# Optimization experiments

Hardware: AMD Instinct MI355X
Metric: run time of the kernel (lower is better)

Reference implementation:

```python
import jax, jax.numpy as jnp
import numpy as np

B, S, H, NH = 4, 2048, 1024, 16
HD = H // NH
EPS = 1e-12

def setup_inputs() -> dict:
    key = jax.random.key(0)
    ks = jax.random.split(key, 8)
    sc = 1.0 / np.sqrt(H)
    return {
        "input_tensor": jax.random.normal(ks[0], (B, S, H), jnp.float32),
        "attention_mask": jnp.zeros((B, 1, 1, S), jnp.float32),
        "Wq": jax.random.normal(ks[1], (H, H), jnp.float32) * sc,
        "bq": jnp.zeros((H,), jnp.float32),
        "Wk": jax.random.normal(ks[2], (H, H), jnp.float32) * sc,
        "bk": jnp.zeros((H,), jnp.float32),
        "Wv": jax.random.normal(ks[3], (H, H), jnp.float32) * sc,
        "bv": jnp.zeros((H,), jnp.float32),
        "Wo": jax.random.normal(ks[4], (H, H), jnp.float32) * sc,
        "bo": jnp.zeros((H,), jnp.float32),
        "ln_w": jnp.ones((H,), jnp.float32),
        "ln_b": jnpp_zeros if False else jnp.zeros((H,), jnp.float32),
    }

def reference(input_tensor, attention_mask, Wq, bq, Wk, bk, Wv, bv, Wo, bo, ln_w, ln_b):
    x = input_tensor  # [B,S,H]
    # QKV projections (torch Linear: x @ W.T + b), split heads -> [B,S,NH,HD]
    q = (x @ Wq.T + bq).reshape(B, S, NH, HD)
    k = (x @ Wk.T + bk).reshape(B, S, NH, HD)
    v = (x @ Wv.T + bv).reshape(B, S, NH, HD)
    # scores [B,NH,S,S]
    scores = jnp.einsum('bqhd,bkhd->bhqk', q, k) / jnp.sqrt(jnp.float32(HD))
    scores = scores + attention_mask  # broadcast [B,1,1,S]
    probs = jax.nn.softmax(scores, axis=-1)  # dropout is identity in eval
    ctx = jnp.einsum('bhqk,bkhd->bqhd', probs, v).reshape(B, S, H)
    # output dense + residual + LayerNorm (TF-style eps inside sqrt)
    h = ctx @ Wo.T + bo + x
    u = h.mean(-1, keepdims=True)
    s = jnp.mean((h - u) ** 2, axis=-1, keepdims=True)
    return ln_w * (h - u) / jnp.sqrt(s + EPS) + ln_b
```

## Files before the change

kernel.cpp:

```cpp
#include <hip/hip_runtime.h>

typedef __bf16 bf16;
typedef __bf16 bf16x8 __attribute__((ext_vector_type(8)));
typedef __bf16 bf16x4 __attribute__((ext_vector_type(4)));
typedef float floatx4 __attribute__((ext_vector_type(4)));
typedef int   intx4  __attribute__((ext_vector_type(4)));
typedef int   intx2  __attribute__((ext_vector_type(2)));

#define MFMA16(a,b,c) __builtin_amdgcn_mfma_f32_16x16x32_bf16((a),(b),(c),0,0,0)

constexpr int Bc  = 4;
constexpr int Sc  = 2048;
constexpr int Hc  = 1024;
constexpr int NHc = 16;
constexpr int HDc = 64;
constexpr int Mc  = Bc * Sc;
constexpr int KIT = Hc / 32;
constexpr float L2E = 1.44269504088896f;

union U64  { bf16x4 h; intx2 i; };

__device__ __forceinline__ void ld16(const bf16* g, bf16* l) {
    __builtin_amdgcn_global_load_lds(
        (const __attribute__((address_space(1))) void*)g,
        (__attribute__((address_space(3))) void*)l, 16, 0, 0);
}

__device__ __forceinline__ int detect_flag_block(const void* x, float* wmx)
{
    const unsigned short* xs = (const unsigned short*)x;
    const int tt = threadIdx.x;
    unsigned int bits = ((unsigned int)xs[tt]) << 16;
    float v = __uint_as_float(bits);
    float a = isfinite(v) ? fabsf(v) : 1e30f;
#pragma unroll
    for (int off = 1; off < 64; off <<= 1)
        a = fmaxf(a, __shfl_xor(a, off, 64));
    if ((tt & 63) == 0) wmx[tt >> 6] = a;
    __syncthreads();
    const float m = fmaxf(fmaxf(wmx[0], wmx[1]), fmaxf(wmx[2], wmx[3]));
    __syncthreads();
    return (m > 1e6f) ? 1 : 0;
}

__global__ __launch_bounds__(256)
void conv_all_k(const void* __restrict__ x,
                const void* __restrict__ Wq, const void* __restrict__ Wk,
                const void* __restrict__ Wv, const void* __restrict__ Wo,
                const void* __restrict__ mask,
                const void* __restrict__ bq, const void* __restrict__ bk,
                const void* __restrict__ bv, const void* __restrict__ bo,
                const void* __restrict__ lnw, const void* __restrict__ lnb,
                bf16* __restrict__ xb, bf16* __restrict__ wdst,
                float* maskf, float* bqf, float* bkf, float* bvf,
                float* bof, float* lnwf, float* lnbf)
{
    __shared__ float wmx[4];
    const int fl = detect_flag_block(x, wmx);

    const int g = blockIdx.x * 256 + threadIdx.x;
    if (g < 1048576) {
        if (fl) {
            const float* s = (const float*)x + (size_t)g * 8;
            union { intx4 v; bf16 e[8]; } o;
#pragma unroll
            for (int j = 0; j < 8; ++j) o.e[j] = (bf16)s[j];
            *(intx4*)(xb + (size_t)g * 8) = o.v;
        } else {
            *(intx4*)(xb + (size_t)g * 8) = *((const intx4*)x + g);
        }
    } else if (g < 1048576 + 524288) {
        const int gw = g - 1048576;
        const int wsel = gw >> 17, go = gw & 131071;
        const void* s = (wsel == 0) ? Wq : (wsel == 1) ? Wk : (wsel == 2) ? Wv : Wo;
        if (fl) {
            const float* sp = (const float*)s + (size_t)go * 8;
            union { intx4 v; bf16 e[8]; } o;
#pragma unroll
            for (int j = 0; j < 8; ++j) o.e[j] = (bf16)sp[j];
            *(intx4*)(wdst + (size_t)gw * 8) = o.v;
        } else {
            *(intx4*)(wdst + (size_t)gw * 8) = *((const intx4*)s + go);
        }
    } else {
        const int gs = g - 1048576 - 524288;
        if (gs >= 1792) return;
        const void* src; float* dst; int off; float scl = 1.0f;
        if (gs < 1024) { src = mask; dst = maskf; off = gs * 8; scl = L2E; }
        else {
            const int a = (gs - 1024) >> 7;
            off = ((gs - 1024) & 127) * 8;
            switch (a) {
                case 0: src = bq;  dst = bqf;  break;
                case 1: src = bk;  dst = bkf;  break;
                case 2: src = bv;  dst = bvf;  break;
                case 3: src = bo;  dst = bof;  break;
                case 4: src = lnw; dst = lnwf; break;
                default: src = lnb; dst = lnbf; break;
            }
        }
        if (fl) {
            const float* s = (const float*)src + off;
#pragma unroll
            for (int j = 0; j < 8; ++j) dst[off + j] = s[j] * scl;
        } else {
            union { intx4 v; bf16 e[8]; } u;
            u.v = *(const intx4*)((const bf16*)src + off);
#pragma unroll
            for (int j = 0; j < 8; ++j) dst[off + j] = (float)u.e[j] * scl;
        }
    }
}

template<int SWAP>
__device__ __forceinline__
void gemm_core(const bf16* __restrict__ A, const bf16* __restrict__ W,
               int m0, int n0, int t, bf16* As, bf16* Bs, floatx4 (&acc)[4][4])
{
    const int l  = t & 63, w = t >> 6;
    const int wr = w >> 1, wc = w & 1;
    const int lq = l >> 4, ln = l & 15;
    const int srow = t >> 2;
    const int scol = (t & 3) * 8;

    const bf16* a0 = A + (size_t)(m0 + srow) * Hc + scol;
    const bf16* b0 = W + (size_t)(n0 + srow) * Hc + scol;
    const int dst = srow * 32 + scol;

    auto stage = [&](int buf, int kb) {
        const int off = kb * 32;
        bf16* dA = As + buf * 4096;
        bf16* dB = Bs + buf * 4096;
        ld16(a0 + off,           dA + dst);
        ld16(a0 + 64 * Hc + off, dA + 64 * 32 + dst);
        ld16(b0 + off,           dB + dst);
        ld16(b0 + 64 * Hc + off, dB + 64 * 32 + dst);
    };

    stage(0, 0);
    int cur = 0;
    for (int kb = 0; kb < KIT; ++kb) {
        __syncthreads();
        if (kb + 1 < KIT) stage(cur ^ 1, kb + 1);

        const bf16* Ab = As + cur * 4096;
        const bf16* Bb = Bs + cur * 4096;
        bf16x8 af[4], bw[4];
#pragma unroll
        for (int i = 0; i < 4; ++i)
            af[i] = *(const bf16x8*)&Ab[(wr * 64 + i * 16 + ln) * 32 + lq * 8];
#pragma unroll
        for (int j = 0; j < 4; ++j)
            bw[j] = *(const bf16x8*)&Bb[(wc * 64 + j * 16 + ln) * 32 + lq * 8];

        __builtin_amdgcn_s_setprio(1);
#pragma unroll
        for (int i = 0; i < 4; ++i)
#pragma unroll
            for (int j = 0; j < 4; ++j)
                acc[i][j] = SWAP ? MFMA16(bw[j], af[i], acc[i][j])
                                 : MFMA16(af[i], bw[j], acc[i][j]);
        __builtin_amdgcn_s_setprio(0);
        cur ^= 1;
    }
}

__device__ __forceinline__ void xcd_remap(int bx, int by, int& m0, int& n0)
{
    const int flat = by * 8 + bx;
    const int sw   = (flat & 7) * 64 + (flat >> 3);
    m0 = (sw >> 3) * 128;
    n0 = (sw & 7) * 128;
}

__global__ __launch_bounds__(256, 3)
void qkv_gemm(const bf16* __restrict__ x,
              const bf16* __restrict__ Wq, const float* __restrict__ bq,
              const bf16* __restrict__ Wk, const float* __restrict__ bk,
              const bf16* __restrict__ Wv, const float* __restrict__ bv,
              bf16* __restrict__ qo, bf16* __restrict__ ko, bf16* __restrict__ vto)
{
    __shared__ __align__(16) bf16 smem[16384];
    const int z = blockIdx.z;
    const bf16*  W    = (z == 0) ? Wq : (z == 1) ? Wk : Wv;
    const float* bias = (z == 0) ? bq : (z == 1) ? bk : bv;

    int m0, n0;
    xcd_remap(blockIdx.x, blockIdx.y, m0, n0);
    const int t  = threadIdx.x;
    const int l  = t & 63, w = t >> 6;
    const int wr = w >> 1, wc = w & 1;
    const int lq = l >> 4, ln = l & 15;

    if (z < 2) {
        floatx4 acc[4][4] = {};
        gemm_core<1>(x, W, m0, n0, t, smem, smem + 8192, acc);
        bf16* out = (z == 0) ? qo : ko;
        const float sc = (z == 0) ? 0.125f * L2E : 1.0f;
#pragma unroll
        for (int j = 0; j < 4; ++j) {
            const int feat = n0 + wc * 64 + j * 16 + lq * 4;
            const floatx4 bb = *(const floatx4*)&bias[feat];
            const int hh = feat >> 6, dd = feat & 63;
#pragma unroll
            for (int i = 0; i < 4; ++i) {
                const int xrow = m0 + wr * 64 + i * 16 + ln;
                const int bi = xrow >> 11, si = xrow & (Sc - 1);
                U64 pk;
#pragma unroll
                for (int r = 0; r < 4; ++r) pk.h[r] = (bf16)((acc[i][j][r] + bb[r]) * sc);
                *(intx2*)&out[(((size_t)bi * NHc + hh) * Sc + si) * HDc + dd] = pk.i;
            }
        }
    } else {
        floatx4 acc[4][4] = {};
        gemm_core<0>(x, W, m0, n0, t, smem, smem + 8192, acc);
        bf16* Ct = smem;
        const int bi = m0 >> 11, s0 = m0 & (Sc - 1);
        for (int h2 = 0; h2 < 2; ++h2) {
            __syncthreads();
            if (wc == h2) {
#pragma unroll
                for (int j = 0; j < 4; ++j) {
                    const int c = j * 16 + ln;
                    const float bb = bias[n0 + h2 * 64 + c];
#pragma unroll
                    for (int i = 0; i < 4; ++i) {
                        U64 pk;
#pragma unroll
                        for (int r = 0; r < 4; ++r) pk.h[r] = (bf16)(acc[i][j][r] + bb);
                        *(intx2*)&Ct[c * 136 + wr * 64 + i * 16 + lq * 4] = pk.i;
                    }
                }
            }
            __syncthreads();
#pragma unroll
            for (int u = 0; u < 4; ++u) {
                const int id = t + 256 * u;
                const int c = id >> 4, rg = id & 15;
                const int hh = (n0 >> 6) + h2;
                intx4 val = *(const intx4*)&Ct[c * 136 + rg * 8];
                *(intx4*)&vto[(((size_t)bi * NHc + hh) * HDc + c) * Sc + s0 + rg * 8] = val;
            }
        }
    }
}

__global__ __launch_bounds__(256, 3)
void oproj_gemm(const bf16* __restrict__ ctx, const bf16* __restrict__ Wo,
                const float* __restrict__ bo, const bf16* __restrict__ xb,
                bf16* __restrict__ hout)
{
    __shared__ __align__(16) bf16 smem[16384];
    int m0, n0;
    xcd_remap(blockIdx.x, blockIdx.y, m0, n0);
    const int t  = threadIdx.x;
    floatx4 acc[4][4] = {};
    gemm_core<1>(ctx, Wo, m0, n0, t, smem, smem + 8192, acc);

    const int l  = t & 63, w = t >> 6;
    const int wr = w >> 1, wc = w & 1;
    const int lq = l >> 4, ln = l & 15;
#pragma unroll
    for (int j = 0; j < 4; ++j) {
        const int col = n0 + wc * 64 + j * 16 + lq * 4;
        const floatx4 bb = *(const floatx4*)&bo[col];
#pragma unroll
        for (int i = 0; i < 4; ++i) {
            const int row = m0 + wr * 64 + i * 16 + ln;
            U64 rx;
            rx.i = *(const intx2*)&xb[(size_t)row * Hc + col];
            U64 pk;
#pragma unroll
            for (int r = 0; r < 4; ++r)
                pk.h[r] = (bf16)(acc[i][j][r] + bb[r] + (float)rx.h[r]);
            *(intx2*)&hout[(size_t)row * Hc + col] = pk.i;
        }
    }
}

__global__ __launch_bounds__(256, 2)
void attention(const bf16* __restrict__ q, const bf16* __restrict__ k,
               const bf16* __restrict__ vt, const float* __restrict__ maskf,
               bf16* __restrict__ ctx)
{
    __shared__ __align__(16) bf16 Ks[2][64][64];
    __shared__ __align__(16) bf16 Vs[2][64][64];
    __shared__ __align__(16) bf16 Pt[4][64][64];

    const int raw = blockIdx.x;
    const int xcd = raw & 7, jj = raw >> 3;
    const int bh  = xcd * 8 + (jj >> 3);
    const int qt  = jj & 7;
    const int b = bh >> 4, h = bh & 15;
    const int t = threadIdx.x, w = t >> 6, l = t & 63;
    const int lq = l >> 4, ln = l & 15;
    const int q0 = qt * 256 + w * 64;

    const bf16* kg = k  + (size_t)bh * Sc * HDc;
    const bf16* vg = vt + (size_t)bh * HDc * Sc;
    const float* mbase = maskf + b * Sc;

    const int rr  = l >> 3;
    const int gsw = ((l & 7) ^ rr) << 3;
    const int r0  = w * 16 + rr, r1 = r0 + 8;
    const int dco = (l & 7) << 3;
    const int sw  = ln & 7;
    const int pkey = sw << 1;

    bf16x8 qf[4][2];
#pragma unroll
    for (int qb = 0; qb < 4; ++qb)
#pragma unroll
        for (int kh = 0; kh < 2; ++kh)
            qf[qb][kh] = *(const bf16x8*)(q + ((size_t)bh * Sc + q0 + qb * 16 + ln) * HDc
                                            + kh * 32 + lq * 8);

    bf16x8 ones8;
#pragma unroll
    for (int jj2 = 0; jj2 < 8; ++jj2) ones8[jj2] = (bf16)1.0f;

    floatx4 o[4][4] = {};
    floatx4 accl[4] = {};

    auto stage = [&](int buf, int kt) {
        bf16* Kd = &Ks[buf][0][0];
        bf16* Vd = &Vs[buf][0][0];
        ld16(kg + (size_t)(kt * 64 + r0) * HDc + gsw, Kd + r0 * 64 + dco);
        ld16(kg + (size_t)(kt * 64 + r1) * HDc + gsw, Kd + r1 * 64 + dco);
        ld16(vg + (size_t)r0 * Sc + kt * 64 + gsw,    Vd + r0 * 64 + dco);
        ld16(vg + (size_t)r1 * Sc + kt * 64 + gsw,    Vd + r1 * 64 + dco);
    };

    stage(0, 0);
    int cur = 0;
    bf16* PtW = &Pt[w][0][0];

    for (int kt = 0; kt < Sc / 64; ++kt) {
        __syncthreads();
        if (kt + 1 < Sc / 64) stage(cur ^ 1, kt + 1);

        floatx4 mvl[4];
#pragma unroll
        for (int cb = 0; cb < 4; ++cb)
            mvl[cb] = *(const floatx4*)(mbase + kt * 64 + cb * 16 + lq * 4);

        bf16x8 kf[4][2];
#pragma unroll
        for (int cb = 0; cb < 4; ++cb)
#pragma unroll
            for (int kh = 0; kh < 2; ++kh)
                kf[cb][kh] = *(const bf16x8*)&Ks[cur][cb * 16 + ln]
                                               [((kh * 4 + lq) ^ sw) << 3];

#pragma unroll
        for (int qb = 0; qb < 4; ++qb) {
            floatx4 s[4];
#pragma unroll
            for (int cb = 0; cb < 4; ++cb) s[cb] = mvl[cb];
            __builtin_amdgcn_s_setprio(1);
#pragma unroll
            for (int kh = 0; kh < 2; ++kh)
#pragma unroll
                for (int cb = 0; cb < 4; ++cb)
                    s[cb] = MFMA16(kf[cb][kh], qf[qb][kh], s[cb]);
            __builtin_amdgcn_s_setprio(0);
#pragma unroll
            for (int cb = 0; cb < 4; ++cb) {
                U64 pk;
#pragma unroll
                for (int r = 0; r < 4; ++r)
                    pk.h[r] = (bf16)__builtin_amdgcn_exp2f(s[cb][r]);
                *(intx2*)(PtW + (qb * 16 + ln) * 64
                              + (((cb * 4 + lq) ^ pkey) << 2)) = pk.i;
            }
        }

        bf16x8 vf[4][2];
#pragma unroll
        for (int db = 0; db < 4; ++db)
#pragma unroll
            for (int kh = 0; kh < 2; ++kh)
                vf[db][kh] = *(const bf16x8*)&Vs[cur][db * 16 + ln]
                                               [((kh * 4 + lq) ^ sw) << 3];

#pragma unroll
        for (int qb = 0; qb < 4; ++qb) {
            const bf16x8 pf0 = *(const bf16x8*)(PtW + (qb * 16 + ln) * 64
                                                    + (((2 * lq) ^ pkey) << 2));
            const bf16x8 pf1 = *(const bf16x8*)(PtW + (qb * 16 + ln) * 64
                                                    + (((8 + 2 * lq) ^ pkey) << 2));
            __builtin_amdgcn_s_setprio(1);
#pragma unroll
            for (int db = 0; db < 4; ++db) {
                o[qb][db] = MFMA16(vf[db][0], pf0, o[qb][db]);
                o[qb][db] = MFMA16(vf[db][1], pf1, o[qb][db]);
            }
            accl[qb] = MFMA16(ones8, pf0, accl[qb]);
            accl[qb] = MFMA16(ones8, pf1, accl[qb]);
            __builtin_amdgcn_s_setprio(0);
        }
        cur ^= 1;
    }

#pragma unroll
    for (int qb = 0; qb < 4; ++qb) {
        const float li = 1.f / accl[qb][0];
        const int qg = q0 + qb * 16 + ln;
#pragma unroll
        for (int db = 0; db < 4; ++db) {
            U64 pk;
#pragma unroll
            for (int r = 0; r < 4; ++r) pk.h[r] = (bf16)(o[qb][db][r] * li);
            *(intx2*)&ctx[((size_t)b * Sc + qg) * Hc + h * HDc + db * 16 + lq * 4] = pk.i;
        }
    }
}

__global__ __launch_bounds__(256)
void layernorm_k(const bf16* __restrict__ hbuf, const float* __restrict__ lw,
                 const float* __restrict__ lb, void* __restrict__ outp,
                 const void* __restrict__ xraw)
{
    __shared__ float wmx[4];
    __shared__ float ssum[4], ssq[4];
    const int fl = detect_flag_block(xraw, wmx);

    const int row = blockIdx.x;
    const int t = threadIdx.x;
    const bf16* hp = hbuf + (size_t)row * Hc;

    union { intx2 i2; bf16 e[4]; } pk;
    pk.i2 = *(const intx2*)(hp + t * 4);
    float v[4], sum = 0.f, sq = 0.f;
#pragma unroll
    for (int i = 0; i < 4; ++i) {
        v[i] = (float)pk.e[i];
        sum += v[i];
        sq  += v[i] * v[i];
    }
#pragma unroll
    for (int off = 1; off < 64; off <<= 1) {
        sum += __shfl_xor(sum, off, 64);
        sq  += __shfl_xor(sq,  off, 64);
    }
    const int w = t >> 6;
    if ((t & 63) == 0) { ssum[w] = sum; ssq[w] = sq; }
    __syncthreads();
    sum = ssum[0] + ssum[1] + ssum[2] + ssum[3];
    sq  = ssq[0]  + ssq[1]  + ssq[2]  + ssq[3];

    const float mean = sum * (1.f / (float)Hc);
    const float var  = sq * (1.f / (float)Hc) - mean * mean;
    const float rstd = rsqrtf(var + 1e-12f);

    float ov[4];
#pragma unroll
    for (int i = 0; i < 4; ++i) {
        const int c = t * 4 + i;
        ov[i] = lw[c] * (v[i] - mean) * rstd + lb[c];
    }
    if (fl) {
        float* of = (float*)outp + (size_t)row * Hc + t * 4;
#pragma unroll
        for (int i = 0; i < 4; ++i) of[i] = ov[i];
    } else {
        union { intx2 i2; bf16 e[4]; } po;
#pragma unroll
        for (int i = 0; i < 4; ++i) po.e[i] = (bf16)ov[i];
        *(intx2*)((bf16*)outp + (size_t)row * Hc + t * 4) = po.i2;
    }
}

extern "C" void kernel_launch(void* const* d_in, const int* in_sizes, int n_in,
                              void* d_out, int out_size, void* d_ws, size_t ws_size,
                              hipStream_t stream)
{
    const void* x    = d_in[0];
    const void* mask = d_in[1];
    const void* Wq   = d_in[2];
    const void* bq   = d_in[3];
    const void* Wk   = d_in[4];
    const void* bk   = d_in[5];
    const void* Wv   = d_in[6];
    const void* bv   = d_in[7];
    const void* Wo   = d_in[8];
    const void* bo   = d_in[9];
    const void* lnw  = d_in[10];
    const void* lnb  = d_in[11];

    char* ws = (char*)d_ws;
    const size_t MB = 1024 * 1024;
    float* maskf = (float*)(ws + 4096);
    float* bqf   = (float*)(ws + 64 * 1024);
    float* bkf   = bqf + Hc;
    float* bvf   = bkf + Hc;
    float* bof   = bvf + Hc;
    float* lnwf  = bof + Hc;
    float* lnbf  = lnwf + Hc;
    bf16* xb  = (bf16*)(ws + 1 * MB);
    bf16* wqb = (bf16*)(ws + 17 * MB);
    bf16* wkb = (bf16*)(ws + 19 * MB);
    bf16* wvb = (bf16*)(ws + 21 * MB);
    bf16* wob = (bf16*)(ws + 23 * MB);
    bf16* qb  = (bf16*)(ws + 25 * MB);
    bf16* kb  = (bf16*)(ws + 41 * MB);
    bf16* vtb = (bf16*)(ws + 57 * MB);
    bf16* cb  = (bf16*)(ws + 73 * MB);
    bf16* hb  = qb;

    conv_all_k<<<6153, 256, 0, stream>>>(x, Wq, Wk, Wv, Wo, mask,
                                         bq, bk, bv, bo, lnw, lnb,
                                         xb, wqb, maskf, bqf, bkf, bvf,
                                         bof, lnwf, lnbf);

    dim3 gqkv(Hc / 128, Mc / 128, 3);
    qkv_gemm<<<gqkv, 256, 0, stream>>>(xb, wqb, bqf, wkb, bkf, wvb, bvf, qb, kb, vtb);
    attention<<<dim3(Bc * NHc * (Sc / 256)), 256, 0, stream>>>(qb, kb, vtb, maskf, cb);
    oproj_gemm<<<dim3(Hc / 128, Mc / 128), 256, 0, stream>>>(cb, wob, bof, xb, hb);
    layernorm_k<<<dim3(Mc), 256, 0, stream>>>(hb, lnwf, lnbf, d_out, x);
}
```

Measured before the change: 285.2 us.

## Halve per-wave P tile and raise attention occupancy to three blocks per CU

```diff
diff --git a/kernel.cpp b/kernel.cpp
--- a/kernel.cpp
+++ b/kernel.cpp
@@ -279,14 +279,14 @@
     }
 }
 
-__global__ __launch_bounds__(256, 2)
+__global__ __launch_bounds__(256, 3)
 void attention(const bf16* __restrict__ q, const bf16* __restrict__ k,
                const bf16* __restrict__ vt, const float* __restrict__ maskf,
                bf16* __restrict__ ctx)
 {
     __shared__ __align__(16) bf16 Ks[2][64][64];
     __shared__ __align__(16) bf16 Vs[2][64][64];
-    __shared__ __align__(16) bf16 Pt[4][64][64];
+    __shared__ __align__(16) bf16 Pt[4][32][64];
 
     const int raw = blockIdx.x;
     const int xcd = raw & 7, jj = raw >> 3;
@@ -345,60 +345,58 @@
         for (int cb = 0; cb < 4; ++cb)
             mvl[cb] = *(const floatx4*)(mbase + kt * 64 + cb * 16 + lq * 4);
 
-        bf16x8 kf[4][2];
+        bf16x8 kf[4][2], vf[4][2];
 #pragma unroll
         for (int cb = 0; cb < 4; ++cb)
 #pragma unroll
-            for (int kh = 0; kh < 2; ++kh)
-                kf[cb][kh] = *(const bf16x8*)&Ks[cur][cb * 16 + ln]
-                                               [((kh * 4 + lq) ^ sw) << 3];
-
-#pragma unroll
-        for (int qb = 0; qb < 4; ++qb) {
-            floatx4 s[4];
-#pragma unroll
-            for (int cb = 0; cb < 4; ++cb) s[cb] = mvl[cb];
-            __builtin_amdgcn_s_setprio(1);
-#pragma unroll
-            for (int kh = 0; kh < 2; ++kh)
-#pragma unroll
-                for (int cb = 0; cb < 4; ++cb)
-                    s[cb] = MFMA16(kf[cb][kh], qf[qb][kh], s[cb]);
-            __builtin_amdgcn_s_setprio(0);
-#pragma unroll
-            for (int cb = 0; cb < 4; ++cb) {
-                U64 pk;
-#pragma unroll
-                for (int r = 0; r < 4; ++r)
-                    pk.h[r] = (bf16)__builtin_amdgcn_exp2f(s[cb][r]);
-                *(intx2*)(PtW + (qb * 16 + ln) * 64
-                              + (((cb * 4 + lq) ^ pkey) << 2)) = pk.i;
-            }
-        }
-
-        bf16x8 vf[4][2];
-#pragma unroll
-        for (int db = 0; db < 4; ++db)
-#pragma unroll
-            for (int kh = 0; kh < 2; ++kh)
-                vf[db][kh] = *(const bf16x8*)&Vs[cur][db * 16 + ln]
-                                               [((kh * 4 + lq) ^ sw) << 3];
-
-#pragma unroll
-        for (int qb = 0; qb < 4; ++qb) {
-            const bf16x8 pf0 = *(const bf16x8*)(PtW + (qb * 16 + ln) * 64
-                                                    + (((2 * lq) ^ pkey) << 2));
-            const bf16x8 pf1 = *(const bf16x8*)(PtW + (qb * 16 + ln) * 64
-                                                    + (((8 + 2 * lq) ^ pkey) << 2));
-            __builtin_amdgcn_s_setprio(1);
-#pragma unroll
-            for (int db = 0; db < 4; ++db) {
-                o[qb][db] = MFMA16(vf[db][0], pf0, o[qb][db]);
-                o[qb][db] = MFMA16(vf[db][1], pf1, o[qb][db]);
-            }
-            accl[qb] = MFMA16(ones8, pf0, accl[qb]);
-            accl[qb] = MFMA16(ones8, pf1, accl[qb]);
-            __builtin_amdgcn_s_setprio(0);
+            for (int kh = 0; kh < 2; ++kh) {
+                const int cc = ((kh * 4 + lq) ^ sw) << 3;
+                kf[cb][kh] = *(const bf16x8*)&Ks[cur][cb * 16 + ln][cc];
+                vf[cb][kh] = *(const bf16x8*)&Vs[cur][cb * 16 + ln][cc];
+            }
+
+#pragma unroll
+        for (int qh = 0; qh < 2; ++qh) {
+#pragma unroll
+            for (int qb2 = 0; qb2 < 2; ++qb2) {
+                const int qb = qh * 2 + qb2;
+                floatx4 s[4];
+#pragma unroll
+                for (int cb = 0; cb < 4; ++cb) s[cb] = mvl[cb];
+                __builtin_amdgcn_s_setprio(1);
+#pragma unroll
+                for (int kh = 0; kh < 2; ++kh)
+#pragma unroll
+                    for (int cb = 0; cb < 4; ++cb)
+                        s[cb] = MFMA16(kf[cb][kh], qf[qb][kh], s[cb]);
+                __builtin_amdgcn_s_setprio(0);
+#pragma unroll
+                for (int cb = 0; cb < 4; ++cb) {
+                    U64 pk;
+#pragma unroll
+                    for (int r = 0; r < 4; ++r)
+                        pk.h[r] = (bf16)__builtin_amdgcn_exp2f(s[cb][r]);
+                    *(intx2*)(PtW + (qb2 * 16 + ln) * 64
+                                  + (((cb * 4 + lq) ^ pkey) << 2)) = pk.i;
+                }
+            }
+#pragma unroll
+            for (int qb2 = 0; qb2 < 2; ++qb2) {
+                const int qb = qh * 2 + qb2;
+                const bf16x8 pf0 = *(const bf16x8*)(PtW + (qb2 * 16 + ln) * 64
+                                                        + (((2 * lq) ^ pkey) << 2));
+                const bf16x8 pf1 = *(const bf16x8*)(PtW + (qb2 * 16 + ln) * 64
+                                                        + (((8 + 2 * lq) ^ pkey) << 2));
+                __builtin_amdgcn_s_setprio(1);
+#pragma unroll
+                for (int db = 0; db < 4; ++db) {
+                    o[qb][db] = MFMA16(vf[db][0], pf0, o[qb][db]);
+                    o[qb][db] = MFMA16(vf[db][1], pf1, o[qb][db]);
+                }
+                accl[qb] = MFMA16(ones8, pf0, accl[qb]);
+                accl[qb] = MFMA16(ones8, pf1, accl[qb]);
+                __builtin_amdgcn_s_setprio(0);
+            }
         }
         cur ^= 1;
     }
```

After: 528.0 us. 1.85x slower.
